# Kernel optimization log

Hardware: AMD Instinct MI355X
Metric: run time of the kernel (lower is better)

## Reference

```python
import jax, jax.numpy as jnp
import numpy as np


def _norm_adj(edge_index, edge_weights, num_nodes):
    """Faithful port of edge_index2norm_adj: dense scatter + self-loops +
    symmetric degree normalization (deg_inv_sqrt is detached in the original)."""
    row, col = edge_index[0], edge_index[1]
    half = edge_weights * 0.5
    adj = jnp.zeros((num_nodes, num_nodes), dtype=edge_weights.dtype)
    adj = adj.at[row, col].add(half)
    adj = adj.at[col, row].add(half)
    adj = adj + jnp.eye(num_nodes, dtype=adj.dtype)
    deg = adj.sum(axis=1)
    deg_inv_sqrt = jnp.where(deg > 0, jax.lax.rsqrt(deg), 0.0)
    deg_inv_sqrt = jax.lax.stop_gradient(deg_inv_sqrt)  # torch.no_grad + detach
    return deg_inv_sqrt[:, None] * adj * deg_inv_sqrt[None, :]


def setup_inputs() -> dict:
    key = jax.random.key(0)
    k1, k2, k3, k4, k5 = jax.random.split(key, 5)
    N, E, D_IN, D_H, D_OUT = 16384, 524288, 64, 64, 16
    x = jax.random.normal(k1, (N, D_IN), dtype=jnp.float32)
    edge_index = jax.random.randint(k2, (2, E), 0, N, dtype=jnp.int64)
    edge_weights = jax.random.uniform(k3, (E,), dtype=jnp.float32)
    W1 = jax.random.normal(k4, (D_IN, D_H), dtype=jnp.float32) / np.sqrt(D_IN)
    b1 = jnp.zeros((D_H,), dtype=jnp.float32)
    W2 = jax.random.normal(k5, (D_H, D_OUT), dtype=jnp.float32) / np.sqrt(D_H)
    b2 = jnp.zeros((D_OUT,), dtype=jnp.float32)
    return {"x": x, "W1": W1, "b1": b1, "W2": W2, "b2": b2,
            "edge_weights": edge_weights, "edge_index": edge_index}


def reference(x, W1, b1, W2, b2, edge_weights, edge_index):
    num_nodes = x.shape[0]
    A = _norm_adj(edge_index, edge_weights, num_nodes)   # [N, N]
    h = jax.nn.relu(A @ (x @ W1) + b1)                   # GCN layer 1
    out = A @ (h @ W2) + b2                              # GCN layer 2 (logits)
    return out
```

## Files before the change

kernel.cpp:

```cpp
#include <hip/hip_runtime.h>

constexpr int TPB   = 256;
constexpr int NMAX  = 16384;
constexpr int CHUNK = 2048;
constexpr int GBMAX = 1024;



__global__ __launch_bounds__(1024) void k_p1(const int* __restrict__ ei,
    const float* __restrict__ ew, int E, int rsh, int NBe, int GB,
    int* __restrict__ bstartT, int* __restrict__ bcntT, int2* __restrict__ tmp) {
    __shared__ int cnt[256];
    __shared__ int curs[256];
    __shared__ int sc[256];
    __shared__ int2 stg[2 * CHUNK];
    int tid = threadIdx.x;
    int b = blockIdx.x;
    int e0 = b * CHUNK;
    int e1 = min(E, e0 + CHUNK);
    if (tid < NBe) cnt[tid] = 0;
    __syncthreads();
    int ea = e0 + tid, ebg = e0 + 1024 + tid;
    int r0 = 0, c0 = 0, r1 = 0, c1 = 0, w0 = 0, w1 = 0;
    bool va = ea < e1, vb = ebg < e1;
    if (va) { r0 = ei[ea];  c0 = ei[E + ea];  w0 = __float_as_int(0.5f * ew[ea]); }
    if (vb) { r1 = ei[ebg]; c1 = ei[E + ebg]; w1 = __float_as_int(0.5f * ew[ebg]); }
    if (va) { atomicAdd(&cnt[r0 >> rsh], 1); atomicAdd(&cnt[c0 >> rsh], 1); }
    if (vb) { atomicAdd(&cnt[r1 >> rsh], 1); atomicAdd(&cnt[c1 >> rsh], 1); }
    __syncthreads();
    int myc = (tid < NBe) ? cnt[tid] : 0;
    if (tid < NBe) sc[tid] = myc;
    __syncthreads();
    for (int off = 1; off < NBe; off <<= 1) {
        int v = 0;
        if (tid < NBe && tid >= off) v = sc[tid - off];
        __syncthreads();
        if (tid < NBe) sc[tid] += v;
        __syncthreads();
    }
    if (tid < NBe) {
        int excl = sc[tid] - myc;
        curs[tid] = excl;
        bstartT[tid * GB + b] = 2 * e0 + excl;
        bcntT[tid * GB + b] = myc;
    }
    __syncthreads();
    int mask = (1 << rsh) - 1;
    if (va) {
        int p = atomicAdd(&curs[r0 >> rsh], 1);
        stg[p] = make_int2(((r0 & mask) << 20) | c0, w0);
        p = atomicAdd(&curs[c0 >> rsh], 1);
        stg[p] = make_int2(((c0 & mask) << 20) | r0, w0);
    }
    if (vb) {
        int p = atomicAdd(&curs[r1 >> rsh], 1);
        stg[p] = make_int2(((r1 & mask) << 20) | c1, w1);
        p = atomicAdd(&curs[c1 >> rsh], 1);
        stg[p] = make_int2(((c1 & mask) << 20) | r1, w1);
    }
    __syncthreads();
    int tot = 2 * (e1 - e0);
    for (int i = tid; i < tot; i += 1024) tmp[2 * e0 + i] = stg[i];
}

__global__ void k_colsum(const int* __restrict__ bcntT, int GB,
                         int* __restrict__ btot) {
    __shared__ int red[TPB / 64];
    int k = blockIdx.x;
    int s = 0;
    for (int b = threadIdx.x; b < GB; b += TPB) s += bcntT[k * GB + b];
    #pragma unroll
    for (int off = 32; off; off >>= 1) s += __shfl_down(s, off, 64);
    int wv = threadIdx.x >> 6;
    if ((threadIdx.x & 63) == 0) red[wv] = s;
    __syncthreads();
    if (threadIdx.x == 0) {
        int t = 0;
        for (int w = 0; w < TPB / 64; ++w) t += red[w];
        btot[k] = t;
    }
}

__global__ __launch_bounds__(1024) void k_p2(const int2* __restrict__ tmp,
    const int* __restrict__ bstartT, const int* __restrict__ bcntT,
    const int* __restrict__ btot, int GB, int rsh, int N, int NBe, int M,
    int2* __restrict__ ent, int* __restrict__ rowptr, float* __restrict__ dis) {
    __shared__ int sco[256];
    __shared__ int ncnt[256];
    __shared__ int nstart[256];
    __shared__ int ncur[256];
    __shared__ float wsum[256];
    int k = blockIdx.x;
    int tid = threadIdx.x;
    int RN = 1 << rsh;
    int n0 = k << rsh;
    int bt = (tid < NBe) ? btot[tid] : 0;
    if (tid < 256) sco[tid] = bt;
    if (tid < RN) { ncnt[tid] = 0; wsum[tid] = 0.f; }
    __syncthreads();
    for (int off = 1; off < 256; off <<= 1) {
        int v = 0;
        if (tid < 256 && tid >= off) v = sco[tid - off];
        __syncthreads();
        if (tid < 256) sco[tid] += v;
        __syncthreads();
    }
    int eb = sco[k] - btot[k];
    int grp = tid >> 2, sub = tid & 3;
    for (int b = grp; b < GB; b += 256) {
        int s = bstartT[k * GB + b];
        int l = bcntT[k * GB + b];
        for (int u = sub; u < l; u += 4) {
            int2 v = tmp[s + u];
            atomicAdd(&ncnt[v.x >> 20], 1);
        }
    }
    __syncthreads();
    int myc = (tid < RN) ? ncnt[tid] : 0;
    if (tid < RN) nstart[tid] = myc;
    __syncthreads();
    for (int off = 1; off < RN; off <<= 1) {
        int v = 0;
        if (tid < RN && tid >= off) v = nstart[tid - off];
        __syncthreads();
        if (tid < RN) nstart[tid] += v;
        __syncthreads();
    }
    if (tid < RN) { nstart[tid] -= myc; ncur[tid] = nstart[tid]; }
    __syncthreads();
    for (int b = grp; b < GB; b += 256) {
        int s = bstartT[k * GB + b];
        int l = bcntT[k * GB + b];
        for (int u = sub; u < l; u += 4) {
            int2 v = tmp[s + u];
            int rl = v.x >> 20;
            int cc = v.x & 0xFFFFF;
            int p = atomicAdd(&ncur[rl], 1);
            ent[eb + p] = make_int2(cc, v.y);
            atomicAdd(&wsum[rl], __int_as_float(v.y));
        }
    }
    __syncthreads();
    if (tid < RN && n0 + tid < N) {
        rowptr[n0 + tid] = eb + nstart[tid];
        dis[n0 + tid] = rsqrtf(1.f + wsum[tid]);
    }
    if (k == 0 && tid == 0) rowptr[N] = M;
}

__global__ void k_init_fb(float* deg, int* counts, int N) {
    int i = blockIdx.x * TPB + threadIdx.x;
    if (i < N) { deg[i] = 1.0f; counts[i] = 0; }
}
__global__ void k_deg_cnt_fb(const int* __restrict__ ei, const float* __restrict__ ew,
                             float* deg, int* counts, int E) {
    int e = blockIdx.x * TPB + threadIdx.x;
    if (e >= E) return;
    int r = ei[e], c = ei[E + e];
    float hw = 0.5f * ew[e];
    unsafeAtomicAdd(&deg[r], hw);
    unsafeAtomicAdd(&deg[c], hw);
    atomicAdd(&counts[r], 1);
    atomicAdd(&counts[c], 1);
}
__global__ void k_rsqrt_fb(float* degdis, int N) {
    int i = blockIdx.x * TPB + threadIdx.x;
    if (i < N) {
        float d = degdis[i];
        degdis[i] = d > 0.f ? rsqrtf(d) : 0.f;
    }
}
__global__ void k_scan_fb(const int* __restrict__ counts, int* __restrict__ rowptr,
                          int* __restrict__ cursor, int N) {
    __shared__ int partial[TPB];
    int tid = threadIdx.x;
    int chunk = (N + TPB - 1) / TPB;
    int begin = tid * chunk;
    int end = begin + chunk; if (end > N) end = N;
    int s = 0;
    for (int i = begin; i < end; ++i) s += counts[i];
    partial[tid] = s;
    __syncthreads();
    for (int off = 1; off < TPB; off <<= 1) {
        int v = partial[tid];
        int add = (tid >= off) ? partial[tid - off] : 0;
        __syncthreads();
        partial[tid] = v + add;
        __syncthreads();
    }
    int base = (tid == 0) ? 0 : partial[tid - 1];
    for (int i = begin; i < end; ++i) {
        rowptr[i] = base; cursor[i] = base;
        base += counts[i];
    }
    if (tid == TPB - 1) rowptr[N] = base;
}
__global__ void k_fill_fb(const int* __restrict__ ei, const float* __restrict__ ew,
                          int* cursor, int2* __restrict__ ent, int E) {
    int e = blockIdx.x * TPB + threadIdx.x;
    if (e >= E) return;
    int r = ei[e], c = ei[E + e];
    int hw = __float_as_int(0.5f * ew[e]);
    int p1 = atomicAdd(&cursor[r], 1);
    ent[p1] = make_int2(c, hw);
    int p2 = atomicAdd(&cursor[c], 1);
    ent[p2] = make_int2(r, hw);
}

__global__ void k_gemm1(const float* __restrict__ X, const float* __restrict__ W,
                        const float* __restrict__ dis, float* __restrict__ Z, int N) {
    __shared__ float Wl[64 * 64];
    int tid = threadIdx.x;
    #pragma unroll
    for (int i = tid; i < 4096; i += TPB) Wl[i] = W[i];
    __syncthreads();
    int row = blockIdx.x * 4 + (tid >> 6);
    int f = tid & 63;
    if (row >= N) return;
    const float* xr = X + row * 64;
    float s = 0.f;
    #pragma unroll
    for (int k = 0; k < 64; ++k) s = fmaf(xr[k], Wl[k * 64 + f], s);
    Z[row * 64 + f] = dis[row] * s;
}

template <int D, bool RELU>
__global__ void k_gather(const float* __restrict__ Z, const int* __restrict__ rowptr,
                         const long long* __restrict__ entq, const float* __restrict__ dis,
                         const float* __restrict__ bias, float* __restrict__ out, int N) {
    constexpr int NPB = TPB / D;
    constexpr int UN = 16;
    int node = blockIdx.x * NPB + threadIdx.x / D;
    int f = threadIdx.x % D;
    int lane = threadIdx.x & 63;
    int base = lane & ~(D - 1);
    if (node >= N) return;
    int j0 = rowptr[node], j1 = rowptr[node + 1];
    float acc = Z[node * D + f];
    long long cur = 0;
    if (j0 < j1) cur = __builtin_nontemporal_load(entq + j0 + f);
    for (int jb = j0; jb < j1; jb += D) {
        long long nxt = cur;
        if (jb + D < j1) nxt = __builtin_nontemporal_load(entq + jb + D + f);
        int ex = (int)cur;
        float ey = __int_as_float((int)(cur >> 32));
        int cnt = j1 - jb; if (cnt > D) cnt = D;
        int k = 0;
        for (; k + UN <= cnt; k += UN) {
            int n[UN]; float w[UN], z[UN];
            #pragma unroll
            for (int u = 0; u < UN; ++u) {
                n[u] = __shfl(ex, base + k + u);
                w[u] = __shfl(ey, base + k + u);
            }
            #pragma unroll
            for (int u = 0; u < UN; ++u) z[u] = Z[n[u] * D + f];
            #pragma unroll
            for (int u = 0; u < UN; ++u) acc = fmaf(w[u], z[u], acc);
        }
        for (; k < cnt; ++k) {
            int n0 = __shfl(ex, base + k);
            float w0 = __shfl(ey, base + k);
            acc = fmaf(w0, Z[n0 * D + f], acc);
        }
        cur = nxt;
    }
    float v = fmaf(dis[node], acc, bias[f]);
    if (RELU) v = v > 0.f ? v : 0.f;
    out[node * D + f] = v;
}

__global__ void k_gemm2(const float* __restrict__ H, const float* __restrict__ W2,
                        const float* __restrict__ dis, float* __restrict__ Z2, int N) {
    __shared__ float Wl[64 * 16];
    int tid = threadIdx.x;
    #pragma unroll
    for (int i = tid; i < 1024; i += TPB) Wl[i] = W2[i];
    __syncthreads();
    int row = blockIdx.x * 16 + (tid >> 4);
    int f = tid & 15;
    if (row >= N) return;
    const float* hr = H + row * 64;
    float s = 0.f;
    #pragma unroll
    for (int k = 0; k < 64; ++k) s = fmaf(hr[k], Wl[k * 16 + f], s);
    Z2[row * 16 + f] = dis[row] * s;
}

extern "C" void kernel_launch(void* const* d_in, const int* in_sizes, int n_in,
                              void* d_out, int out_size, void* d_ws, size_t ws_size,
                              hipStream_t stream) {
    const float* x  = (const float*)d_in[0];
    const float* W1 = (const float*)d_in[1];
    const float* b1 = (const float*)d_in[2];
    const float* W2 = (const float*)d_in[3];
    const float* b2 = (const float*)d_in[4];
    const float* ew = (const float*)d_in[5];
    const int*   ei = (const int*)d_in[6];

    const int N = in_sizes[0] / 64;
    const int E = in_sizes[5];
    const int M = 2 * E;

    int rsh = 0;
    while ((256 << rsh) < N) ++rsh;
    const int NBe = (N + (1 << rsh) - 1) >> rsh;
    const int GB  = (E + CHUNK - 1) / CHUNK;

    char* ws = (char*)d_ws;
    size_t off = 0;
    auto alloc = [&](size_t bytes) -> void* {
        void* p = ws + off;
        off += (bytes + 255) & ~(size_t)255;
        return p;
    };
    float* dis     = (float*)alloc((size_t)N * 4);
    int*   counts  = (int*)alloc((size_t)N * 4);
    int*   rowptr  = (int*)alloc(((size_t)N + 1) * 4);
    int*   cursor  = (int*)alloc((size_t)N * 4);
    int2*  ent     = (int2*)alloc(((size_t)M + 64) * 8);
    int*   bstartT = (int*)alloc((size_t)GB * NBe * 4);
    int*   bcntT   = (int*)alloc((size_t)GB * NBe * 4);
    int*   btot    = (int*)alloc(((size_t)NBe + 1) * 4);
    float* Z1      = (float*)alloc((size_t)N * 64 * 4);
    float* H       = (float*)alloc((size_t)N * 64 * 4);
    float* Z2      = (float*)alloc((size_t)N * 16 * 4);
    (void)ws_size; (void)n_in; (void)out_size;

    int2* tmp = (int2*)Z1;

    float* out = (float*)d_out;

    if (N <= NMAX && GB <= GBMAX && (size_t)16 * E <= (size_t)512 * N) {
        k_p1<<<GB, 1024, 0, stream>>>(ei, ew, E, rsh, NBe, GB, bstartT, bcntT, tmp);
        k_colsum<<<NBe, TPB, 0, stream>>>(bcntT, GB, btot);
        k_p2<<<NBe, 1024, 0, stream>>>(tmp, bstartT, bcntT, btot, GB, rsh, N, NBe, M,
                                       ent, rowptr, dis);
    } else {
        k_init_fb<<<(N + TPB - 1) / TPB, TPB, 0, stream>>>(dis, counts, N);
        k_deg_cnt_fb<<<(E + TPB - 1) / TPB, TPB, 0, stream>>>(ei, ew, dis, counts, E);
        k_rsqrt_fb<<<(N + TPB - 1) / TPB, TPB, 0, stream>>>(dis, N);
        k_scan_fb<<<1, TPB, 0, stream>>>(counts, rowptr, cursor, N);
        k_fill_fb<<<(E + TPB - 1) / TPB, TPB, 0, stream>>>(ei, ew, cursor, ent, E);
    }

    k_gemm1<<<(N + 3) / 4, TPB, 0, stream>>>(x, W1, dis, Z1, N);
    k_gather<64, true><<<(N + 3) / 4, TPB, 0, stream>>>(Z1, rowptr, (const long long*)ent,
                                                        dis, b1, H, N);
    k_gemm2<<<(N + 15) / 16, TPB, 0, stream>>>(H, W2, dis, Z2, N);
    k_gather<16, false><<<(N + 15) / 16, TPB, 0, stream>>>(Z2, rowptr, (const long long*)ent,
                                                           dis, b2, out, N);
}
```

Measured before the change: 156.1 us.

## Fuse layer-1 gather with W2 projection and fold column-sum into p2

Layer-1 aggregation now applies bias, ReLU and the 64x16 W2 projection in-register through wave shuffles and writes Z2 directly. This removes the H intermediate round trip and the separate gemm2 launch. The k_colsum kernel is also dropped: every p2 block recomputes the bucket totals with shared-memory atomics over the whole bcntT table. That saves a launch but repeats the full-table reduction in each of the NBe blocks.

Measured after the change: 211.4 us. 1.35x slower.

```diff
diff --git a/kernel.cpp b/kernel.cpp
--- a/kernel.cpp
+++ b/kernel.cpp
@@ -63,28 +63,11 @@
     for (int i = tid; i < tot; i += 1024) tmp[2 * e0 + i] = stg[i];
 }
 
-__global__ void k_colsum(const int* __restrict__ bcntT, int GB,
-                         int* __restrict__ btot) {
-    __shared__ int red[TPB / 64];
-    int k = blockIdx.x;
-    int s = 0;
-    for (int b = threadIdx.x; b < GB; b += TPB) s += bcntT[k * GB + b];
-    #pragma unroll
-    for (int off = 32; off; off >>= 1) s += __shfl_down(s, off, 64);
-    int wv = threadIdx.x >> 6;
-    if ((threadIdx.x & 63) == 0) red[wv] = s;
-    __syncthreads();
-    if (threadIdx.x == 0) {
-        int t = 0;
-        for (int w = 0; w < TPB / 64; ++w) t += red[w];
-        btot[k] = t;
-    }
-}
-
 __global__ __launch_bounds__(1024) void k_p2(const int2* __restrict__ tmp,
     const int* __restrict__ bstartT, const int* __restrict__ bcntT,
-    const int* __restrict__ btot, int GB, int rsh, int N, int NBe, int M,
+    int GB, int rsh, int N, int NBe, int M,
     int2* __restrict__ ent, int* __restrict__ rowptr, float* __restrict__ dis) {
+    __shared__ int btl[256];
     __shared__ int sco[256];
     __shared__ int ncnt[256];
     __shared__ int nstart[256];
@@ -94,9 +77,16 @@
     int tid = threadIdx.x;
     int RN = 1 << rsh;
     int n0 = k << rsh;
-    int bt = (tid < NBe) ? btot[tid] : 0;
+    if (tid < 256) btl[tid] = 0;
+    if (tid < RN) { ncnt[tid] = 0; wsum[tid] = 0.f; }
+    __syncthreads();
+    int totTab = NBe * GB;
+    for (int i = tid; i < totTab; i += 1024) {
+        atomicAdd(&btl[i / GB], bcntT[i]);
+    }
+    __syncthreads();
+    int bt = (tid < 256) ? btl[tid] : 0;
     if (tid < 256) sco[tid] = bt;
-    if (tid < RN) { ncnt[tid] = 0; wsum[tid] = 0.f; }
     __syncthreads();
     for (int off = 1; off < 256; off <<= 1) {
         int v = 0;
@@ -105,7 +95,7 @@
         if (tid < 256) sco[tid] += v;
         __syncthreads();
     }
-    int eb = sco[k] - btot[k];
+    int eb = sco[k] - btl[k];
     int grp = tid >> 2, sub = tid & 3;
     for (int b = grp; b < GB; b += 256) {
         int s = bstartT[k * GB + b];
@@ -222,6 +212,64 @@
     #pragma unroll
     for (int k = 0; k < 64; ++k) s = fmaf(xr[k], Wl[k * 64 + f], s);
     Z[row * 64 + f] = dis[row] * s;
+}
+
+__global__ void k_gatherL1(const float* __restrict__ Z, const int* __restrict__ rowptr,
+                           const long long* __restrict__ entq, const float* __restrict__ dis,
+                           const float* __restrict__ b1, const float* __restrict__ W2,
+                           float* __restrict__ Z2, int N) {
+    constexpr int UN = 16;
+    __shared__ float W2s[64 * 16];
+    int tid = threadIdx.x;
+    #pragma unroll
+    for (int i = tid; i < 1024; i += TPB) W2s[i] = W2[i];
+    __syncthreads();
+    int node = blockIdx.x * 4 + (tid >> 6);
+    int f = tid & 63;
+    if (node >= N) return;
+    int j0 = rowptr[node], j1 = rowptr[node + 1];
+    float acc = Z[node * 64 + f];
+    long long cur = 0;
+    if (j0 < j1) cur = __builtin_nontemporal_load(entq + j0 + f);
+    for (int jb = j0; jb < j1; jb += 64) {
+        long long nxt = cur;
+        if (jb + 64 < j1) nxt = __builtin_nontemporal_load(entq + jb + 64 + f);
+        int ex = (int)cur;
+        float ey = __int_as_float((int)(cur >> 32));
+        int cnt = j1 - jb; if (cnt > 64) cnt = 64;
+        int k = 0;
+        for (; k + UN <= cnt; k += UN) {
+            int n[UN]; float w[UN], z[UN];
+            #pragma unroll
+            for (int u = 0; u < UN; ++u) {
+                n[u] = __shfl(ex, k + u);
+                w[u] = __shfl(ey, k + u);
+            }
+            #pragma unroll
+            for (int u = 0; u < UN; ++u) z[u] = Z[n[u] * 64 + f];
+            #pragma unroll
+            for (int u = 0; u < UN; ++u) acc = fmaf(w[u], z[u], acc);
+        }
+        for (; k < cnt; ++k) {
+            int n0 = __shfl(ex, k);
+            float w0 = __shfl(ey, k);
+            acc = fmaf(w0, Z[n0 * 64 + f], acc);
+        }
+        cur = nxt;
+    }
+    float h = fmaf(dis[node], acc, b1[f]);
+    h = h > 0.f ? h : 0.f;
+    int g = f & 15, seg = f >> 4;
+    float p = 0.f;
+    #pragma unroll
+    for (int i = 0; i < 16; ++i) {
+        int ff = seg * 16 + i;
+        float hv = __shfl(h, ff);
+        p = fmaf(hv, W2s[ff * 16 + g], p);
+    }
+    p += __shfl_xor(p, 16);
+    p += __shfl_xor(p, 32);
+    if (seg == 0) Z2[node * 16 + g] = dis[node] * p;
 }
 
 template <int D, bool RELU>
@@ -270,23 +318,6 @@
     out[node * D + f] = v;
 }
 
-__global__ void k_gemm2(const float* __restrict__ H, const float* __restrict__ W2,
-                        const float* __restrict__ dis, float* __restrict__ Z2, int N) {
-    __shared__ float Wl[64 * 16];
-    int tid = threadIdx.x;
-    #pragma unroll
-    for (int i = tid; i < 1024; i += TPB) Wl[i] = W2[i];
-    __syncthreads();
-    int row = blockIdx.x * 16 + (tid >> 4);
-    int f = tid & 15;
-    if (row >= N) return;
-    const float* hr = H + row * 64;
-    float s = 0.f;
-    #pragma unroll
-    for (int k = 0; k < 64; ++k) s = fmaf(hr[k], Wl[k * 16 + f], s);
-    Z2[row * 16 + f] = dis[row] * s;
-}
-
 extern "C" void kernel_launch(void* const* d_in, const int* in_sizes, int n_in,
                               void* d_out, int out_size, void* d_ws, size_t ws_size,
                               hipStream_t stream) {
@@ -321,11 +352,10 @@
     int2*  ent     = (int2*)alloc(((size_t)M + 64) * 8);
     int*   bstartT = (int*)alloc((size_t)GB * NBe * 4);
     int*   bcntT   = (int*)alloc((size_t)GB * NBe * 4);
-    int*   btot    = (int*)alloc(((size_t)NBe + 1) * 4);
     float* Z1      = (float*)alloc((size_t)N * 64 * 4);
-    float* H       = (float*)alloc((size_t)N * 64 * 4);
+    float* scratch = (float*)alloc((size_t)N * 64 * 4);
     float* Z2      = (float*)alloc((size_t)N * 16 * 4);
-    (void)ws_size; (void)n_in; (void)out_size;
+    (void)ws_size; (void)n_in; (void)out_size; (void)scratch;
 
     int2* tmp = (int2*)Z1;
 
@@ -333,8 +363,7 @@
 
     if (N <= NMAX && GB <= GBMAX && (size_t)16 * E <= (size_t)512 * N) {
         k_p1<<<GB, 1024, 0, stream>>>(ei, ew, E, rsh, NBe, GB, bstartT, bcntT, tmp);
-        k_colsum<<<NBe, TPB, 0, stream>>>(bcntT, GB, btot);
-        k_p2<<<NBe, 1024, 0, stream>>>(tmp, bstartT, bcntT, btot, GB, rsh, N, NBe, M,
+        k_p2<<<NBe, 1024, 0, stream>>>(tmp, bstartT, bcntT, GB, rsh, N, NBe, M,
                                        ent, rowptr, dis);
     } else {
         k_init_fb<<<(N + TPB - 1) / TPB, TPB, 0, stream>>>(dis, counts, N);
@@ -345,9 +374,8 @@
     }
 
     k_gemm1<<<(N + 3) / 4, TPB, 0, stream>>>(x, W1, dis, Z1, N);
-    k_gather<64, true><<<(N + 3) / 4, TPB, 0, stream>>>(Z1, rowptr, (const long long*)ent,
-                                                        dis, b1, H, N);
-    k_gemm2<<<(N + 15) / 16, TPB, 0, stream>>>(H, W2, dis, Z2, N);
+    k_gatherL1<<<(N + 3) / 4, TPB, 0, stream>>>(Z1, rowptr, (const long long*)ent,
+                                                dis, b1, W2, Z2, N);
     k_gather<16, false><<<(N + 15) / 16, TPB, 0, stream>>>(Z2, rowptr, (const long long*)ent,
                                                            dis, b2, out, N);
 }
```
